# Performance work log

Measured on AMD Instinct MI355X. Metric: run time of the kernel, lower is better.

Reference implementation:

```python
import jax, jax.numpy as jnp
import numpy as np

NU = 100000  # num user nodes
NI = 100000  # num item nodes
E = 1600000  # edges per edge type
L = 100000   # labeled edges
H = 128      # hidden_channels
EPS = 1e-12  # F.normalize eps


def sage_conv(x_src, x_dst, edge_index, w_l, b_l, w_r, num_dst):
    """PyG SAGEConv, mean aggregation, normalize=True.
    w_l, w_r: [H, H] stored as [in, out]; lin_r has no bias."""
    src, dst = edge_index[0], edge_index[1]
    msg_sum = jax.ops.segment_sum(x_src[src], dst, num_segments=num_dst)  # [num_dst, H]
    cnt = jax.ops.segment_sum(jnp.ones((src.shape[0],), x_src.dtype), dst, num_segments=num_dst)
    mean = msg_sum / jnp.maximum(cnt, 1.0)[:, None]
    out = mean @ w_l + b_l + x_dst @ w_r
    norm = jnp.sqrt(jnp.sum(out * out, axis=-1, keepdims=True))
    return out / jnp.maximum(norm, EPS)


def setup_inputs() -> dict:
    key = jax.random.key(0)
    ks = jax.random.split(key, 20)
    s = 1.0 / np.sqrt(H)
    d = {
        'emb_user': jax.random.normal(ks[0], (NU, H), jnp.float32),
        'emb_item': jax.random.normal(ks[1], (NI, H), jnp.float32),
        'edge_rates': jax.random.randint(ks[2], (2, E), 0, 100000, jnp.int32),
        'edge_rev': jax.random.randint(ks[3], (2, E), 0, 100000, jnp.int32),
        'edge_label_index': jax.random.randint(ks[4], (2, L), 0, 100000, jnp.int32),
    }
    names = ['w1l_rates', 'w1r_rates', 'w1l_rev', 'w1r_rev',
             'w2l_rates', 'w2r_rates', 'w2l_rev', 'w2r_rev']
    for i, n in enumerate(names):
        d[n] = jax.random.uniform(ks[5 + i], (H, H), jnp.float32, -s, s)
    for i, n in enumerate(['b1_rates', 'b1_rev', 'b2_rates', 'b2_rev']):
        d[n] = jax.random.uniform(ks[13 + i], (H,), jnp.float32, -s, s)
    return d


def reference(emb_user, emb_item, edge_rates, edge_rev, edge_label_index,
              w1l_rates, w1r_rates, w1l_rev, w1r_rev,
              w2l_rates, w2r_rates, w2l_rev, w2r_rev,
              b1_rates, b1_rev, b2_rates, b2_rev):
    xu, xi = emb_user, emb_item
    # layer 1: each node type receives exactly one edge type (HeteroConv mean is identity)
    xi1 = sage_conv(xu, xi, edge_rates, w1l_rates, b1_rates, w1r_rates, NI)
    xu1 = sage_conv(xi, xu, edge_rev, w1l_rev, b1_rev, w1r_rev, NU)
    xu1 = jax.nn.relu(xu1)  # dropout is identity in eval mode
    xi1 = jax.nn.relu(xi1)
    # layer 2
    xi2 = sage_conv(xu1, xi1, edge_rates, w2l_rates, b2_rates, w2r_rates, NI)
    xu2 = sage_conv(xi1, xu1, edge_rev, w2l_rev, b2_rev, w2r_rev, NU)
    xu2 = jax.nn.relu(xu2)
    xi2 = jax.nn.relu(xi2)
    # classifier: dot(user[src], item[dst])
    x_src = xu2[edge_label_index[0]]
    x_dst = xi2[edge_label_index[1]]
    return jnp.sum(x_src * x_dst, axis=-1)
```

## Files before the change

kernel.cpp:

```cpp
#include <hip/hip_runtime.h>
#include <hip/hip_bf16.h>

#define NUM_U 100000
#define NUM_I 100000
#define NE    1600000
#define NL    100000
#define CAP   48
#define NBIN  391
#define BINCAP 4608
#define ROUND  4096
#define PB    391

typedef __attribute__((ext_vector_type(4))) float floatx4;
typedef __attribute__((ext_vector_type(8))) short shortx8;
typedef __attribute__((ext_vector_type(4))) unsigned uintx4;
typedef unsigned long long u64;

__device__ __forceinline__ float bf_lo(unsigned v) { return __uint_as_float(v << 16); }
__device__ __forceinline__ float bf_hi(unsigned v) { return __uint_as_float(v & 0xffff0000u); }

__device__ __forceinline__ unsigned pack_bf16x2(float lo, float hi) {
    __hip_bfloat16 l = __float2bfloat16(lo);
    __hip_bfloat16 h = __float2bfloat16(hi);
    unsigned short ul = *(unsigned short*)&l;
    unsigned short uh = *(unsigned short*)&h;
    return (unsigned)ul | ((unsigned)uh << 16);
}

__device__ __forceinline__ int clampi(int x, int hi) {
    return min(max(x, 0), hi - 1);
}

__global__ void prep1_kernel(
    const float* __restrict__ w1l_rates, const float* __restrict__ w1r_rates,
    const float* __restrict__ w1l_rev,   const float* __restrict__ w1r_rev,
    const float* __restrict__ w2l_rates, const float* __restrict__ w2r_rates,
    const float* __restrict__ w2l_rev,   const float* __restrict__ w2r_rev,
    short* __restrict__ Bt, int* __restrict__ bin_cursor,
    float* __restrict__ tailp, int ntail) {
    int idx = blockIdx.x * blockDim.x + threadIdx.x;
    if (idx < 2 * NBIN) bin_cursor[idx] = 0;
    if (idx < 4 * 32768) {
        int which = idx >> 15;
        int r = idx & 32767;
        int n = r >> 8;
        int k = r & 255;
        const float *wl, *wr;
        switch (which) {
            case 0:  wl = w1l_rates; wr = w1r_rates; break;
            case 1:  wl = w1l_rev;   wr = w1r_rev;   break;
            case 2:  wl = w2l_rates; wr = w2r_rates; break;
            default: wl = w2l_rev;   wr = w2r_rev;   break;
        }
        float v = (k < 128) ? wl[k * 128 + n] : wr[(k - 128) * 128 + n];
        __hip_bfloat16 b = __float2bfloat16(v);
        Bt[idx] = *(const short*)&b;
    } else {
        int t = idx - 4 * 32768;
        if (t < ntail) tailp[t] = 0.0f;
    }
}

__global__ __launch_bounds__(256) void prep2_kernel(
    const int* __restrict__ edges0, const int* __restrict__ edges1,
    u64* __restrict__ bd0, u64* __restrict__ bd1, int* __restrict__ cur,
    const float* __restrict__ emb_u, const float* __restrict__ emb_i,
    unsigned* __restrict__ xu, unsigned* __restrict__ xi) {
    __shared__ int hist[NBIN];
    __shared__ int prefix[NBIN];
    __shared__ int gbase[NBIN];
    __shared__ __align__(16) u64 sorted[ROUND];

    if (blockIdx.x >= 2 * PB) {
        int i = (blockIdx.x - 2 * PB) * blockDim.x + threadIdx.x;
        const int nu = NUM_U * 64;
        if (i < nu) {
            float2 v = ((const float2*)emb_u)[i];
            xu[i] = pack_bf16x2(v.x, v.y);
        } else if (i < nu + NUM_I * 64) {
            int j = i - nu;
            float2 v = ((const float2*)emb_i)[j];
            xi[j] = pack_bf16x2(v.x, v.y);
        }
        return;
    }

    const int type = (blockIdx.x >= PB) ? 1 : 0;
    const int* edges = type ? edges1 : edges0;
    u64* bin_data = type ? bd1 : bd0;
    int* bin_cursor = cur + type * NBIN;
    const int blk  = blockIdx.x - type * PB;
    const int tid  = threadIdx.x;
    const int lane = tid & 63;
    const int wv   = tid >> 6;
    const int base = blk * ROUND;

    for (int k = tid; k < NBIN; k += 256) hist[k] = 0;
    __syncthreads();

    int mybin[16], myrank[16], mysrc[16], mydst[16];
#pragma unroll
    for (int r = 0; r < 16; r++) {
        int i = base + r * 256 + tid;
        mybin[r] = -1;
        if (i < NE) {
            mysrc[r] = clampi(edges[i], NUM_U);
            mydst[r] = clampi(edges[i + NE], NUM_I);
            mybin[r] = mydst[r] >> 8;
            myrank[r] = atomicAdd(&hist[mybin[r]], 1);
        }
    }
    __syncthreads();

    if (wv == 0) {
        int carry = 0;
        for (int c = 0; c < NBIN; c += 64) {
            int idx = c + lane;
            int h = (idx < NBIN) ? hist[idx] : 0;
            int v = h;
            for (int o = 1; o < 64; o <<= 1) {
                int t = __shfl_up(v, o);
                if (lane >= o) v += t;
            }
            if (idx < NBIN) prefix[idx] = v - h + carry;
            carry += __shfl(v, 63);
        }
    }
    __syncthreads();

#pragma unroll
    for (int r = 0; r < 16; r++) {
        if (mybin[r] >= 0) {
            int j = prefix[mybin[r]] + myrank[r];
            sorted[j] = ((u64)(unsigned)mydst[r] << 32) | (unsigned)mysrc[r];
        }
    }
    __syncthreads();

    for (int b = tid; b < NBIN; b += 256) {
        int cnt = hist[b];
        gbase[b] = (cnt > 0) ? atomicAdd(&bin_cursor[b], cnt) : 0;
    }
    __syncthreads();

    int total = min(ROUND, NE - base);
    for (int j = tid; j < total; j += 256) {
        u64 e = sorted[j];
        int b = (int)(e >> 40);
        int pos = gbase[b] + (j - prefix[b]);
        if (pos < BINCAP)
            bin_data[(size_t)b * BINCAP + pos] = e;
    }
}

__global__ __launch_bounds__(256) void binscatter2_kernel(
    const u64* __restrict__ bd0, const u64* __restrict__ bd1, const int* __restrict__ cur,
    int* __restrict__ deg0, int* __restrict__ bucket0,
    int* __restrict__ deg1, int* __restrict__ bucket1) {
    __shared__ int lbucket[256 * CAP];
    __shared__ int ldeg[256];
    const int type = (blockIdx.x >= NBIN) ? 1 : 0;
    const int b = blockIdx.x - type * NBIN;
    const u64* bin_data = type ? bd1 : bd0;
    int* deg = type ? deg1 : deg0;
    int* bucket = type ? bucket1 : bucket0;
    const int tid = threadIdx.x;
    const int dstbase = b << 8;
    const int n_dst = NUM_I;

    ldeg[tid] = 0;
    __syncthreads();

    int count = min(cur[type * NBIN + b], BINCAP);
    for (int j = tid; j < count; j += 256) {
        u64 e = bin_data[(size_t)b * BINCAP + j];
        int src = (int)(unsigned)e;
        int dl = ((int)(e >> 32)) & 255;
        int pos = atomicAdd(&ldeg[dl], 1);
        if (pos < CAP) lbucket[dl * CAP + pos] = src;
    }
    __syncthreads();

    if (dstbase + tid < n_dst) deg[dstbase + tid] = ldeg[tid];
    int limit = min(256, n_dst - dstbase) * CAP;
    for (int k = tid; k < limit; k += 256)
        bucket[(size_t)dstbase * CAP + k] = lbucket[k];
}

__global__ __launch_bounds__(256) void agg2_kernel(
    const int* __restrict__ degA, const int* __restrict__ bucketA,
    const unsigned* __restrict__ xA, unsigned* __restrict__ outA,
    const int* __restrict__ degB, const int* __restrict__ bucketB,
    const unsigned* __restrict__ xB, unsigned* __restrict__ outB) {
    const int bid = blockIdx.x;
    const int g = bid & 7;
    const int typeB = (g >= 4);
    const int gidx = (bid >> 3) * 4 + (g & 3);
    const int node = gidx * 4 + (threadIdx.x >> 6);
    const int lane = threadIdx.x & 63;
    if (node >= NUM_I) return;

    const int* deg; const int* bucket; const unsigned* xb; unsigned* mo;
    if (!typeB) { deg = degA; bucket = bucketA; xb = xA; mo = outA; }
    else        { deg = degB; bucket = bucketB; xb = xB; mo = outB; }

    int d = __builtin_nontemporal_load(&deg[node]);
    int cnt = min(d, CAP);
    int srcs = (lane < cnt) ? __builtin_nontemporal_load(&bucket[(size_t)node * CAP + lane]) : 0;
    float a0 = 0.f, a1 = 0.f;
    int e = 0;
    for (; e + 8 <= cnt; e += 8) {
        int s0 = __builtin_amdgcn_readlane(srcs, e + 0);
        int s1 = __builtin_amdgcn_readlane(srcs, e + 1);
        int s2 = __builtin_amdgcn_readlane(srcs, e + 2);
        int s3 = __builtin_amdgcn_readlane(srcs, e + 3);
        int s4 = __builtin_amdgcn_readlane(srcs, e + 4);
        int s5 = __builtin_amdgcn_readlane(srcs, e + 5);
        int s6 = __builtin_amdgcn_readlane(srcs, e + 6);
        int s7 = __builtin_amdgcn_readlane(srcs, e + 7);
        unsigned v0 = xb[(size_t)s0 * 64 + lane];
        unsigned v1 = xb[(size_t)s1 * 64 + lane];
        unsigned v2 = xb[(size_t)s2 * 64 + lane];
        unsigned v3 = xb[(size_t)s3 * 64 + lane];
        unsigned v4 = xb[(size_t)s4 * 64 + lane];
        unsigned v5 = xb[(size_t)s5 * 64 + lane];
        unsigned v6 = xb[(size_t)s6 * 64 + lane];
        unsigned v7 = xb[(size_t)s7 * 64 + lane];
        a0 += bf_lo(v0) + bf_lo(v1) + bf_lo(v2) + bf_lo(v3)
            + bf_lo(v4) + bf_lo(v5) + bf_lo(v6) + bf_lo(v7);
        a1 += bf_hi(v0) + bf_hi(v1) + bf_hi(v2) + bf_hi(v3)
            + bf_hi(v4) + bf_hi(v5) + bf_hi(v6) + bf_hi(v7);
    }
    for (; e + 4 <= cnt; e += 4) {
        int s0 = __builtin_amdgcn_readlane(srcs, e + 0);
        int s1 = __builtin_amdgcn_readlane(srcs, e + 1);
        int s2 = __builtin_amdgcn_readlane(srcs, e + 2);
        int s3 = __builtin_amdgcn_readlane(srcs, e + 3);
        unsigned v0 = xb[(size_t)s0 * 64 + lane];
        unsigned v1 = xb[(size_t)s1 * 64 + lane];
        unsigned v2 = xb[(size_t)s2 * 64 + lane];
        unsigned v3 = xb[(size_t)s3 * 64 + lane];
        a0 += bf_lo(v0) + bf_lo(v1) + bf_lo(v2) + bf_lo(v3);
        a1 += bf_hi(v0) + bf_hi(v1) + bf_hi(v2) + bf_hi(v3);
    }
    for (; e < cnt; e++) {
        int s0 = __builtin_amdgcn_readlane(srcs, e);
        unsigned v0 = xb[(size_t)s0 * 64 + lane];
        a0 += bf_lo(v0); a1 += bf_hi(v0);
    }
    float scale = 1.0f / (float)max(d, 1);
    __builtin_nontemporal_store(pack_bf16x2(a0 * scale, a1 * scale),
                                &mo[(size_t)node * 64 + lane]);
}

__global__ __launch_bounds__(256) void gemm2r_kernel(
    const unsigned* __restrict__ meanA, unsigned* __restrict__ xA,
    const short* __restrict__ BtA, const float* __restrict__ biasA,
    const unsigned* __restrict__ meanB, unsigned* __restrict__ xB,
    const short* __restrict__ BtB, const float* __restrict__ biasB,
    int nblocksA) {
    __shared__ float rowsum[128][2];

    const int half = (blockIdx.x >= nblocksA) ? 1 : 0;
    const unsigned* meanb = half ? meanB : meanA;
    const unsigned* xdstb = half ? xB : xA;
    unsigned* outb = half ? xB : xA;
    const short* Bt = half ? BtB : BtA;
    const float* bias = half ? biasB : biasA;
    const int rb = (blockIdx.x - half * nblocksA) * 128;
    const int n_rows = NUM_I;

    const int tid  = threadIdx.x;
    const int lane = tid & 63;
    const int wv   = tid >> 6;
    const int wm   = wv >> 1;
    const int wn   = wv & 1;
    const int l15  = lane & 15;
    const int lq   = lane >> 4;

    floatx4 acc[4][4];
#pragma unroll
    for (int nt = 0; nt < 4; nt++) {
        float b = bias[wn * 64 + nt * 16 + l15];
#pragma unroll
        for (int mt = 0; mt < 4; mt++) acc[mt][nt] = (floatx4){b, b, b, b};
    }

    for (int kt = 0; kt < 4; kt++) {
        const unsigned* srcbuf = (kt < 2) ? meanb : xdstb;
        const int kbase_u = (kt & 1) * 32;
        uintx4 a8[4][2];
#pragma unroll
        for (int mt = 0; mt < 4; mt++) {
#pragma unroll
            for (int kk2 = 0; kk2 < 2; kk2++) {
                int grow = rb + wm * 64 + mt * 16 + l15;
                uintx4 v = (uintx4){0u, 0u, 0u, 0u};
                if (grow < n_rows)
                    v = *(const uintx4*)(srcbuf + (size_t)grow * 64 + kbase_u + kk2 * 16 + lq * 4);
                a8[mt][kk2] = v;
            }
        }
#pragma unroll
        for (int kk2 = 0; kk2 < 2; kk2++) {
            shortx8 bfr[4];
#pragma unroll
            for (int nt = 0; nt < 4; nt++) {
                int col = wn * 64 + nt * 16 + l15;
                int kg = kt * 64 + kk2 * 32 + lq * 8;
                bfr[nt] = *(const shortx8*)(Bt + col * 256 + kg);
            }
#pragma unroll
            for (int mt = 0; mt < 4; mt++)
#pragma unroll
                for (int nt = 0; nt < 4; nt++)
                    acc[mt][nt] = __builtin_amdgcn_mfma_f32_16x16x32_bf16(
                        *(const shortx8*)&a8[mt][kk2], bfr[nt], acc[mt][nt], 0, 0, 0);
        }
    }

#pragma unroll
    for (int mt = 0; mt < 4; mt++) {
#pragma unroll
        for (int r = 0; r < 4; r++) {
            float p = 0.f;
#pragma unroll
            for (int nt = 0; nt < 4; nt++) { float x = acc[mt][nt][r]; p += x * x; }
            for (int o = 1; o < 16; o <<= 1) p += __shfl_xor(p, o);
            if (l15 == 0) rowsum[wm * 64 + mt * 16 + lq * 4 + r][wn] = p;
        }
    }
    __syncthreads();

#pragma unroll
    for (int mt = 0; mt < 4; mt++) {
#pragma unroll
        for (int r = 0; r < 4; r++) {
            int row_l = wm * 64 + mt * 16 + lq * 4 + r;
            int grow = rb + row_l;
            float s = rowsum[row_l][0] + rowsum[row_l][1];
            float inv = 1.f / fmaxf(sqrtf(s), 1e-12f);
#pragma unroll
            for (int nt = 0; nt < 4; nt++) {
                float v = fmaxf(acc[mt][nt][r] * inv, 0.f);
                float vnb = __shfl_xor(v, 1);
                if (grow < n_rows && (l15 & 1) == 0) {
                    int colpair = (wn * 64 + nt * 16 + l15) >> 1;
                    outb[(size_t)grow * 64 + colpair] = pack_bf16x2(v, vnb);
                }
            }
        }
    }
}

__global__ __launch_bounds__(256) void classifier_kernel(
    const unsigned* __restrict__ xu, const unsigned* __restrict__ xi,
    const int* __restrict__ eli, float* __restrict__ out, int nL) {
    int wave = (blockIdx.x * blockDim.x + threadIdx.x) >> 6;
    int lane = threadIdx.x & 63;
    if (wave >= nL) return;
    int su = clampi(eli[wave], NUM_U);
    int di = clampi(eli[wave + nL], NUM_I);
    unsigned a = xu[(size_t)su * 64 + lane];
    unsigned b = xi[(size_t)di * 64 + lane];
    float p = bf_lo(a) * bf_lo(b) + bf_hi(a) * bf_hi(b);
    for (int o = 32; o; o >>= 1) p += __shfl_xor(p, o);
    if (lane == 0) __builtin_nontemporal_store(p, &out[wave]);
}

extern "C" void kernel_launch(void* const* d_in, const int* in_sizes, int n_in,
                              void* d_out, int out_size, void* d_ws, size_t ws_size,
                              hipStream_t stream) {
    const float* emb_user = (const float*)d_in[0];
    const float* emb_item = (const float*)d_in[1];
    const int* edge_rates = (const int*)d_in[2];
    const int* edge_rev   = (const int*)d_in[3];
    const int* eli        = (const int*)d_in[4];
    const float* b1_rates = (const float*)d_in[13];
    const float* b1_rev   = (const float*)d_in[14];
    const float* b2_rates = (const float*)d_in[15];
    const float* b2_rev   = (const float*)d_in[16];

    char* p = (char*)d_ws;
    auto alloc = [&](size_t bytes) -> void* {
        void* q = (void*)p;
        p += (bytes + 511) & ~(size_t)511;
        return q;
    };
    int* deg_rates    = (int*)alloc((size_t)NUM_I * 4);
    int* bucket_rates = (int*)alloc((size_t)NUM_I * CAP * 4);
    int* deg_rev      = (int*)alloc((size_t)NUM_U * 4);
    int* bucket_rev   = (int*)alloc((size_t)NUM_U * CAP * 4);
    unsigned* meanI = (unsigned*)alloc((size_t)NUM_I * 64 * 4);
    unsigned* meanU = (unsigned*)alloc((size_t)NUM_U * 64 * 4);
    unsigned* xi    = (unsigned*)alloc((size_t)NUM_I * 64 * 4);
    unsigned* xu    = (unsigned*)alloc((size_t)NUM_U * 64 * 4);
    short* Bt = (short*)alloc((size_t)4 * 32768 * 2);
    int* bin_cursor = (int*)alloc((size_t)2 * NBIN * 4);
    u64* bd0 = (u64*)meanI;
    u64* bd1 = (u64*)meanU;

    const int gemmBlocks = (NUM_I + 127) / 128;
    const int agg2Blocks = 2 * ((NUM_I + 3) / 4);
    const int conv2Blocks = ((NUM_U + NUM_I) * 64 + 255) / 256;

    const int ntail = (out_size > NL) ? (out_size - NL) : 0;
    const int prep1Blocks = 512 + (ntail + 255) / 256;
    const int prep2Blocks = 2 * PB + conv2Blocks;

    prep1_kernel<<<prep1Blocks, 256, 0, stream>>>(
        (const float*)d_in[5], (const float*)d_in[6],
        (const float*)d_in[7], (const float*)d_in[8],
        (const float*)d_in[9], (const float*)d_in[10],
        (const float*)d_in[11], (const float*)d_in[12], Bt, bin_cursor,
        (float*)d_out + NL, ntail);
    prep2_kernel<<<prep2Blocks, 256, 0, stream>>>(edge_rates, edge_rev, bd0, bd1, bin_cursor,
                                                  emb_user, emb_item, xu, xi);
    binscatter2_kernel<<<2 * NBIN, 256, 0, stream>>>(bd0, bd1, bin_cursor,
                                                     deg_rates, bucket_rates,
                                                     deg_rev, bucket_rev);

    agg2_kernel<<<agg2Blocks, 256, 0, stream>>>(deg_rates, bucket_rates, xu, meanI,
                                                deg_rev, bucket_rev, xi, meanU);
    gemm2r_kernel<<<2 * gemmBlocks, 256, 0, stream>>>(meanI, xi, Bt + 0 * 32768, b1_rates,
                                                      meanU, xu, Bt + 1 * 32768, b1_rev,
                                                      gemmBlocks);

    agg2_kernel<<<agg2Blocks, 256, 0, stream>>>(deg_rates, bucket_rates, xu, meanI,
                                                deg_rev, bucket_rev, xi, meanU);
    gemm2r_kernel<<<2 * gemmBlocks, 256, 0, stream>>>(meanI, xi, Bt + 2 * 32768, b2_rates,
                                                      meanU, xu, Bt + 3 * 32768, b2_rev,
                                                      gemmBlocks);

    classifier_kernel<<<(NL * 64 + 255) / 256, 256, 0, stream>>>(xu, xi, eli,
                                                                 (float*)d_out, NL);
}
```

Baseline: 638.1 us.

## Interleave aggregation and GEMM blocks in one kernel to overlap gather and MFMA phases

Merges the neighbour-mean gather and the SAGE linear/normalize GEMM into one kernel whose blocks are interleaved (one GEMM block per 17). The four aggregations and four GEMMs are reordered into a five-launch software pipeline, so each GEMM runs alongside the next aggregation, using ping-pong feature buffers. The GEMM tile drops to 64 rows with a full 128-column wave tile, which removes the shared-memory row-sum reduction. The embedding conversion is split out from the edge partition kernel. This trades extra buffers and careful dependency ordering for overlap of the memory-bound gather with compute-bound MFMA work.

Result: slower. 794.6 us (+24.5%).

```diff
diff --git a/kernel.cpp b/kernel.cpp
--- a/kernel.cpp
+++ b/kernel.cpp
@@ -10,6 +10,9 @@
 #define BINCAP 4608
 #define ROUND  4096
 #define PB    391
+#define NAGG  25000
+#define NGEMM 1563
+#define ILV   17
 
 typedef __attribute__((ext_vector_type(4))) float floatx4;
 typedef __attribute__((ext_vector_type(8))) short shortx8;
@@ -61,29 +64,27 @@
     }
 }
 
-__global__ __launch_bounds__(256) void prep2_kernel(
+__global__ void conv2_kernel(const float* __restrict__ emb_u, const float* __restrict__ emb_i,
+                             unsigned* __restrict__ xu, unsigned* __restrict__ xi) {
+    int i = blockIdx.x * blockDim.x + threadIdx.x;
+    const int nu = NUM_U * 64;
+    if (i < nu) {
+        float2 v = ((const float2*)emb_u)[i];
+        xu[i] = pack_bf16x2(v.x, v.y);
+    } else if (i < nu + NUM_I * 64) {
+        int j = i - nu;
+        float2 v = ((const float2*)emb_i)[j];
+        xi[j] = pack_bf16x2(v.x, v.y);
+    }
+}
+
+__global__ __launch_bounds__(256) void partition2_kernel(
     const int* __restrict__ edges0, const int* __restrict__ edges1,
-    u64* __restrict__ bd0, u64* __restrict__ bd1, int* __restrict__ cur,
-    const float* __restrict__ emb_u, const float* __restrict__ emb_i,
-    unsigned* __restrict__ xu, unsigned* __restrict__ xi) {
+    u64* __restrict__ bd0, u64* __restrict__ bd1, int* __restrict__ cur) {
     __shared__ int hist[NBIN];
     __shared__ int prefix[NBIN];
     __shared__ int gbase[NBIN];
     __shared__ __align__(16) u64 sorted[ROUND];
-
-    if (blockIdx.x >= 2 * PB) {
-        int i = (blockIdx.x - 2 * PB) * blockDim.x + threadIdx.x;
-        const int nu = NUM_U * 64;
-        if (i < nu) {
-            float2 v = ((const float2*)emb_u)[i];
-            xu[i] = pack_bf16x2(v.x, v.y);
-        } else if (i < nu + NUM_I * 64) {
-            int j = i - nu;
-            float2 v = ((const float2*)emb_i)[j];
-            xi[j] = pack_bf16x2(v.x, v.y);
-        }
-        return;
-    }
 
     const int type = (blockIdx.x >= PB) ? 1 : 0;
     const int* edges = type ? edges1 : edges0;
@@ -187,22 +188,73 @@
         bucket[(size_t)dstbase * CAP + k] = lbucket[k];
 }
 
-__global__ __launch_bounds__(256) void agg2_kernel(
-    const int* __restrict__ degA, const int* __restrict__ bucketA,
-    const unsigned* __restrict__ xA, unsigned* __restrict__ outA,
-    const int* __restrict__ degB, const int* __restrict__ bucketB,
-    const unsigned* __restrict__ xB, unsigned* __restrict__ outB) {
+__global__ __launch_bounds__(256, 8) void ag_kernel(
+    int nAgg, int nGemm,
+    const int* __restrict__ deg, const int* __restrict__ bucket,
+    const unsigned* __restrict__ xsrc, unsigned* __restrict__ mout,
+    const unsigned* __restrict__ gmean, const unsigned* __restrict__ gxdst,
+    const short* __restrict__ gBt, const float* __restrict__ gbias,
+    unsigned* __restrict__ gout) {
     const int bid = blockIdx.x;
-    const int g = bid & 7;
-    const int typeB = (g >= 4);
-    const int gidx = (bid >> 3) * 4 + (g & 3);
-    const int node = gidx * 4 + (threadIdx.x >> 6);
-    const int lane = threadIdx.x & 63;
+    int gemmIdx = -1, aggIdx = -1;
+    if (nGemm == 0) aggIdx = bid;
+    else if (nAgg == 0) gemmIdx = bid;
+    else {
+        int q = bid / ILV, r = bid - q * ILV;
+        if (r == 0 && q < nGemm) gemmIdx = q;
+        else aggIdx = bid - min(q + (r ? 1 : 0), nGemm);
+    }
+
+    const int tid  = threadIdx.x;
+    const int lane = tid & 63;
+    const int wv   = tid >> 6;
+    const int l15  = lane & 15;
+    const int lq   = lane >> 4;
+
+    if (gemmIdx >= 0) {
+        const int rb = gemmIdx * 64;
+        floatx4 acc[8];
+#pragma unroll
+        for (int nt = 0; nt < 8; nt++) {
+            float b = gbias[nt * 16 + l15];
+            acc[nt] = (floatx4){b, b, b, b};
+        }
+        const int grow = rb + wv * 16 + l15;
+#pragma unroll
+        for (int kt = 0; kt < 8; kt++) {
+            const unsigned* srcbuf = (kt < 4) ? gmean : gxdst;
+            uintx4 av = (uintx4){0u, 0u, 0u, 0u};
+            if (grow < NUM_I)
+                av = *(const uintx4*)(srcbuf + (size_t)grow * 64 + (kt & 3) * 16 + lq * 4);
+            shortx8 af = *(const shortx8*)&av;
+#pragma unroll
+            for (int nt = 0; nt < 8; nt++) {
+                shortx8 bfr = *(const shortx8*)(gBt + (nt * 16 + l15) * 256 + kt * 32 + lq * 8);
+                acc[nt] = __builtin_amdgcn_mfma_f32_16x16x32_bf16(af, bfr, acc[nt], 0, 0, 0);
+            }
+        }
+#pragma unroll
+        for (int r = 0; r < 4; r++) {
+            float p = 0.f;
+#pragma unroll
+            for (int nt = 0; nt < 8; nt++) { float x = acc[nt][r]; p += x * x; }
+            p += __shfl_xor(p, 1); p += __shfl_xor(p, 2);
+            p += __shfl_xor(p, 4); p += __shfl_xor(p, 8);
+            float inv = 1.f / fmaxf(sqrtf(p), 1e-12f);
+            int grow_out = rb + wv * 16 + lq * 4 + r;
+#pragma unroll
+            for (int nt = 0; nt < 8; nt++) {
+                float v = fmaxf(acc[nt][r] * inv, 0.f);
+                float vnb = __shfl_xor(v, 1);
+                if (grow_out < NUM_I && (l15 & 1) == 0)
+                    gout[(size_t)grow_out * 64 + ((nt * 16 + l15) >> 1)] = pack_bf16x2(v, vnb);
+            }
+        }
+        return;
+    }
+
+    const int node = aggIdx * 4 + wv;
     if (node >= NUM_I) return;
-
-    const int* deg; const int* bucket; const unsigned* xb; unsigned* mo;
-    if (!typeB) { deg = degA; bucket = bucketA; xb = xA; mo = outA; }
-    else        { deg = degB; bucket = bucketB; xb = xB; mo = outB; }
 
     int d = __builtin_nontemporal_load(&deg[node]);
     int cnt = min(d, CAP);
@@ -218,14 +270,14 @@
         int s5 = __builtin_amdgcn_readlane(srcs, e + 5);
         int s6 = __builtin_amdgcn_readlane(srcs, e + 6);
         int s7 = __builtin_amdgcn_readlane(srcs, e + 7);
-        unsigned v0 = xb[(size_t)s0 * 64 + lane];
-        unsigned v1 = xb[(size_t)s1 * 64 + lane];
-        unsigned v2 = xb[(size_t)s2 * 64 + lane];
-        unsigned v3 = xb[(size_t)s3 * 64 + lane];
-        unsigned v4 = xb[(size_t)s4 * 64 + lane];
-        unsigned v5 = xb[(size_t)s5 * 64 + lane];
-        unsigned v6 = xb[(size_t)s6 * 64 + lane];
-        unsigned v7 = xb[(size_t)s7 * 64 + lane];
+        unsigned v0 = xsrc[(size_t)s0 * 64 + lane];
+        unsigned v1 = xsrc[(size_t)s1 * 64 + lane];
+        unsigned v2 = xsrc[(size_t)s2 * 64 + lane];
+        unsigned v3 = xsrc[(size_t)s3 * 64 + lane];
+        unsigned v4 = xsrc[(size_t)s4 * 64 + lane];
+        unsigned v5 = xsrc[(size_t)s5 * 64 + lane];
+        unsigned v6 = xsrc[(size_t)s6 * 64 + lane];
+        unsigned v7 = xsrc[(size_t)s7 * 64 + lane];
         a0 += bf_lo(v0) + bf_lo(v1) + bf_lo(v2) + bf_lo(v3)
             + bf_lo(v4) + bf_lo(v5) + bf_lo(v6) + bf_lo(v7);
         a1 += bf_hi(v0) + bf_hi(v1) + bf_hi(v2) + bf_hi(v3)
@@ -236,121 +288,21 @@
         int s1 = __builtin_amdgcn_readlane(srcs, e + 1);
         int s2 = __builtin_amdgcn_readlane(srcs, e + 2);
         int s3 = __builtin_amdgcn_readlane(srcs, e + 3);
-        unsigned v0 = xb[(size_t)s0 * 64 + lane];
-        unsigned v1 = xb[(size_t)s1 * 64 + lane];
-        unsigned v2 = xb[(size_t)s2 * 64 + lane];
-        unsigned v3 = xb[(size_t)s3 * 64 + lane];
+        unsigned v0 = xsrc[(size_t)s0 * 64 + lane];
+        unsigned v1 = xsrc[(size_t)s1 * 64 + lane];
+        unsigned v2 = xsrc[(size_t)s2 * 64 + lane];
+        unsigned v3 = xsrc[(size_t)s3 * 64 + lane];
         a0 += bf_lo(v0) + bf_lo(v1) + bf_lo(v2) + bf_lo(v3);
         a1 += bf_hi(v0) + bf_hi(v1) + bf_hi(v2) + bf_hi(v3);
     }
     for (; e < cnt; e++) {
         int s0 = __builtin_amdgcn_readlane(srcs, e);
-        unsigned v0 = xb[(size_t)s0 * 64 + lane];
+        unsigned v0 = xsrc[(size_t)s0 * 64 + lane];
         a0 += bf_lo(v0); a1 += bf_hi(v0);
     }
     float scale = 1.0f / (float)max(d, 1);
     __builtin_nontemporal_store(pack_bf16x2(a0 * scale, a1 * scale),
-                                &mo[(size_t)node * 64 + lane]);
-}
-
-__global__ __launch_bounds__(256) void gemm2r_kernel(
-    const unsigned* __restrict__ meanA, unsigned* __restrict__ xA,
-    const short* __restrict__ BtA, const float* __restrict__ biasA,
-    const unsigned* __restrict__ meanB, unsigned* __restrict__ xB,
-    const short* __restrict__ BtB, const float* __restrict__ biasB,
-    int nblocksA) {
-    __shared__ float rowsum[128][2];
-
-    const int half = (blockIdx.x >= nblocksA) ? 1 : 0;
-    const unsigned* meanb = half ? meanB : meanA;
-    const unsigned* xdstb = half ? xB : xA;
-    unsigned* outb = half ? xB : xA;
-    const short* Bt = half ? BtB : BtA;
-    const float* bias = half ? biasB : biasA;
-    const int rb = (blockIdx.x - half * nblocksA) * 128;
-    const int n_rows = NUM_I;
-
-    const int tid  = threadIdx.x;
-    const int lane = tid & 63;
-    const int wv   = tid >> 6;
-    const int wm   = wv >> 1;
-    const int wn   = wv & 1;
-    const int l15  = lane & 15;
-    const int lq   = lane >> 4;
-
-    floatx4 acc[4][4];
-#pragma unroll
-    for (int nt = 0; nt < 4; nt++) {
-        float b = bias[wn * 64 + nt * 16 + l15];
-#pragma unroll
-        for (int mt = 0; mt < 4; mt++) acc[mt][nt] = (floatx4){b, b, b, b};
-    }
-
-    for (int kt = 0; kt < 4; kt++) {
-        const unsigned* srcbuf = (kt < 2) ? meanb : xdstb;
-        const int kbase_u = (kt & 1) * 32;
-        uintx4 a8[4][2];
-#pragma unroll
-        for (int mt = 0; mt < 4; mt++) {
-#pragma unroll
-            for (int kk2 = 0; kk2 < 2; kk2++) {
-                int grow = rb + wm * 64 + mt * 16 + l15;
-                uintx4 v = (uintx4){0u, 0u, 0u, 0u};
-                if (grow < n_rows)
-                    v = *(const uintx4*)(srcbuf + (size_t)grow * 64 + kbase_u + kk2 * 16 + lq * 4);
-                a8[mt][kk2] = v;
-            }
-        }
-#pragma unroll
-        for (int kk2 = 0; kk2 < 2; kk2++) {
-            shortx8 bfr[4];
-#pragma unroll
-            for (int nt = 0; nt < 4; nt++) {
-                int col = wn * 64 + nt * 16 + l15;
-                int kg = kt * 64 + kk2 * 32 + lq * 8;
-                bfr[nt] = *(const shortx8*)(Bt + col * 256 + kg);
-            }
-#pragma unroll
-            for (int mt = 0; mt < 4; mt++)
-#pragma unroll
-                for (int nt = 0; nt < 4; nt++)
-                    acc[mt][nt] = __builtin_amdgcn_mfma_f32_16x16x32_bf16(
-                        *(const shortx8*)&a8[mt][kk2], bfr[nt], acc[mt][nt], 0, 0, 0);
-        }
-    }
-
-#pragma unroll
-    for (int mt = 0; mt < 4; mt++) {
-#pragma unroll
-        for (int r = 0; r < 4; r++) {
-            float p = 0.f;
-#pragma unroll
-            for (int nt = 0; nt < 4; nt++) { float x = acc[mt][nt][r]; p += x * x; }
-            for (int o = 1; o < 16; o <<= 1) p += __shfl_xor(p, o);
-            if (l15 == 0) rowsum[wm * 64 + mt * 16 + lq * 4 + r][wn] = p;
-        }
-    }
-    __syncthreads();
-
-#pragma unroll
-    for (int mt = 0; mt < 4; mt++) {
-#pragma unroll
-        for (int r = 0; r < 4; r++) {
-            int row_l = wm * 64 + mt * 16 + lq * 4 + r;
-            int grow = rb + row_l;
-            float s = rowsum[row_l][0] + rowsum[row_l][1];
-            float inv = 1.f / fmaxf(sqrtf(s), 1e-12f);
-#pragma unroll
-            for (int nt = 0; nt < 4; nt++) {
-                float v = fmaxf(acc[mt][nt][r] * inv, 0.f);
-                float vnb = __shfl_xor(v, 1);
-                if (grow < n_rows && (l15 & 1) == 0) {
-                    int colpair = (wn * 64 + nt * 16 + l15) >> 1;
-                    outb[(size_t)grow * 64 + colpair] = pack_bf16x2(v, vnb);
-                }
-            }
-        }
-    }
+                                &mout[(size_t)node * 64 + lane]);
 }
 
 __global__ __launch_bounds__(256) void classifier_kernel(
@@ -391,22 +343,22 @@
     int* bucket_rates = (int*)alloc((size_t)NUM_I * CAP * 4);
     int* deg_rev      = (int*)alloc((size_t)NUM_U * 4);
     int* bucket_rev   = (int*)alloc((size_t)NUM_U * CAP * 4);
-    unsigned* meanI = (unsigned*)alloc((size_t)NUM_I * 64 * 4);
-    unsigned* meanU = (unsigned*)alloc((size_t)NUM_U * 64 * 4);
-    unsigned* xi    = (unsigned*)alloc((size_t)NUM_I * 64 * 4);
-    unsigned* xu    = (unsigned*)alloc((size_t)NUM_U * 64 * 4);
+    unsigned* M1  = (unsigned*)alloc((size_t)NUM_I * 64 * 4);
+    unsigned* M2  = (unsigned*)alloc((size_t)NUM_U * 64 * 4);
+    unsigned* xi0 = (unsigned*)alloc((size_t)NUM_I * 64 * 4);
+    unsigned* xu0 = (unsigned*)alloc((size_t)NUM_U * 64 * 4);
+    unsigned* xi1 = (unsigned*)alloc((size_t)NUM_I * 64 * 4);
+    unsigned* xu1 = (unsigned*)alloc((size_t)NUM_U * 64 * 4);
     short* Bt = (short*)alloc((size_t)4 * 32768 * 2);
     int* bin_cursor = (int*)alloc((size_t)2 * NBIN * 4);
-    u64* bd0 = (u64*)meanI;
-    u64* bd1 = (u64*)meanU;
-
-    const int gemmBlocks = (NUM_I + 127) / 128;
-    const int agg2Blocks = 2 * ((NUM_I + 3) / 4);
+    u64* bd0 = (u64*)M1;
+    u64* bd1 = (u64*)M2;
+    unsigned* M3 = xi0;
+
     const int conv2Blocks = ((NUM_U + NUM_I) * 64 + 255) / 256;
-
     const int ntail = (out_size > NL) ? (out_size - NL) : 0;
     const int prep1Blocks = 512 + (ntail + 255) / 256;
-    const int prep2Blocks = 2 * PB + conv2Blocks;
+    const int agBlocks = NAGG + NGEMM;
 
     prep1_kernel<<<prep1Blocks, 256, 0, stream>>>(
         (const float*)d_in[5], (const float*)d_in[6],
@@ -414,24 +366,28 @@
         (const float*)d_in[9], (const float*)d_in[10],
         (const float*)d_in[11], (const float*)d_in[12], Bt, bin_cursor,
         (float*)d_out + NL, ntail);
-    prep2_kernel<<<prep2Blocks, 256, 0, stream>>>(edge_rates, edge_rev, bd0, bd1, bin_cursor,
-                                                  emb_user, emb_item, xu, xi);
+    conv2_kernel<<<conv2Blocks, 256, 0, stream>>>(emb_user, emb_item, xu0, xi0);
+    partition2_kernel<<<2 * PB, 256, 0, stream>>>(edge_rates, edge_rev, bd0, bd1, bin_cursor);
     binscatter2_kernel<<<2 * NBIN, 256, 0, stream>>>(bd0, bd1, bin_cursor,
                                                      deg_rates, bucket_rates,
                                                      deg_rev, bucket_rev);
 
-    agg2_kernel<<<agg2Blocks, 256, 0, stream>>>(deg_rates, bucket_rates, xu, meanI,
-                                                deg_rev, bucket_rev, xi, meanU);
-    gemm2r_kernel<<<2 * gemmBlocks, 256, 0, stream>>>(meanI, xi, Bt + 0 * 32768, b1_rates,
-                                                      meanU, xu, Bt + 1 * 32768, b1_rev,
-                                                      gemmBlocks);
-
-    agg2_kernel<<<agg2Blocks, 256, 0, stream>>>(deg_rates, bucket_rates, xu, meanI,
-                                                deg_rev, bucket_rev, xi, meanU);
-    gemm2r_kernel<<<2 * gemmBlocks, 256, 0, stream>>>(meanI, xi, Bt + 2 * 32768, b2_rates,
-                                                      meanU, xu, Bt + 3 * 32768, b2_rev,
-                                                      gemmBlocks);
-
-    classifier_kernel<<<(NL * 64 + 255) / 256, 256, 0, stream>>>(xu, xi, eli,
+    ag_kernel<<<NAGG, 256, 0, stream>>>(NAGG, 0,
+        deg_rates, bucket_rates, xu0, M1,
+        M1, xi0, Bt, b1_rates, xi1);
+    ag_kernel<<<agBlocks, 256, 0, stream>>>(NAGG, NGEMM,
+        deg_rev, bucket_rev, xi0, M2,
+        M1, xi0, Bt + 0 * 32768, b1_rates, xi1);
+    ag_kernel<<<agBlocks, 256, 0, stream>>>(NAGG, NGEMM,
+        deg_rev, bucket_rev, xi1, M3,
+        M2, xu0, Bt + 1 * 32768, b1_rev, xu1);
+    ag_kernel<<<agBlocks, 256, 0, stream>>>(NAGG, NGEMM,
+        deg_rates, bucket_rates, xu1, M1,
+        M3, xu1, Bt + 3 * 32768, b2_rev, xu0);
+    ag_kernel<<<NGEMM, 256, 0, stream>>>(0, NGEMM,
+        deg_rates, bucket_rates, xu1, M1,
+        M1, xi1, Bt + 2 * 32768, b2_rates, xi0);
+
+    classifier_kernel<<<(NL * 64 + 255) / 256, 256, 0, stream>>>(xu0, xi0, eli,
                                                                  (float*)d_out, NL);
 }
```

## Use per-wave full-row GEMM tiles and split conversion out of partition kernel

Applied to the files above, without the earlier changes.

The GEMM+normalize kernel is retiled so each wave owns 16 full rows across all 128 output columns. The row L2 norm can then be reduced entirely with in-wave shuffles, removing the shared-memory rowsum and block barrier, at the cost of less A-fragment reuse across N and more B loads per wave. Separately, the embedding fp32-to-bf16 conversion is moved out of the edge-partition kernel into its own launch. This adds a kernel launch but gives the partition kernel a simpler, uniform grid.

New measurement: 692.1 us. 8.5% more time.

```diff
diff --git a/kernel.cpp b/kernel.cpp
--- a/kernel.cpp
+++ b/kernel.cpp
@@ -61,29 +61,27 @@
     }
 }
 
-__global__ __launch_bounds__(256) void prep2_kernel(
+__global__ void conv2_kernel(const float* __restrict__ emb_u, const float* __restrict__ emb_i,
+                             unsigned* __restrict__ xu, unsigned* __restrict__ xi) {
+    int i = blockIdx.x * blockDim.x + threadIdx.x;
+    const int nu = NUM_U * 64;
+    if (i < nu) {
+        float2 v = ((const float2*)emb_u)[i];
+        xu[i] = pack_bf16x2(v.x, v.y);
+    } else if (i < nu + NUM_I * 64) {
+        int j = i - nu;
+        float2 v = ((const float2*)emb_i)[j];
+        xi[j] = pack_bf16x2(v.x, v.y);
+    }
+}
+
+__global__ __launch_bounds__(256) void partition2_kernel(
     const int* __restrict__ edges0, const int* __restrict__ edges1,
-    u64* __restrict__ bd0, u64* __restrict__ bd1, int* __restrict__ cur,
-    const float* __restrict__ emb_u, const float* __restrict__ emb_i,
-    unsigned* __restrict__ xu, unsigned* __restrict__ xi) {
+    u64* __restrict__ bd0, u64* __restrict__ bd1, int* __restrict__ cur) {
     __shared__ int hist[NBIN];
     __shared__ int prefix[NBIN];
     __shared__ int gbase[NBIN];
     __shared__ __align__(16) u64 sorted[ROUND];
-
-    if (blockIdx.x >= 2 * PB) {
-        int i = (blockIdx.x - 2 * PB) * blockDim.x + threadIdx.x;
-        const int nu = NUM_U * 64;
-        if (i < nu) {
-            float2 v = ((const float2*)emb_u)[i];
-            xu[i] = pack_bf16x2(v.x, v.y);
-        } else if (i < nu + NUM_I * 64) {
-            int j = i - nu;
-            float2 v = ((const float2*)emb_i)[j];
-            xi[j] = pack_bf16x2(v.x, v.y);
-        }
-        return;
-    }
 
     const int type = (blockIdx.x >= PB) ? 1 : 0;
     const int* edges = type ? edges1 : edges0;
@@ -253,102 +251,61 @@
                                 &mo[(size_t)node * 64 + lane]);
 }
 
-__global__ __launch_bounds__(256) void gemm2r_kernel(
+__global__ __launch_bounds__(256) void gemmw_kernel(
     const unsigned* __restrict__ meanA, unsigned* __restrict__ xA,
     const short* __restrict__ BtA, const float* __restrict__ biasA,
     const unsigned* __restrict__ meanB, unsigned* __restrict__ xB,
     const short* __restrict__ BtB, const float* __restrict__ biasB,
     int nblocksA) {
-    __shared__ float rowsum[128][2];
-
     const int half = (blockIdx.x >= nblocksA) ? 1 : 0;
     const unsigned* meanb = half ? meanB : meanA;
-    const unsigned* xdstb = half ? xB : xA;
-    unsigned* outb = half ? xB : xA;
+    unsigned* xb = half ? xB : xA;
     const short* Bt = half ? BtB : BtA;
     const float* bias = half ? biasB : biasA;
-    const int rb = (blockIdx.x - half * nblocksA) * 128;
-    const int n_rows = NUM_I;
-
-    const int tid  = threadIdx.x;
-    const int lane = tid & 63;
-    const int wv   = tid >> 6;
-    const int wm   = wv >> 1;
-    const int wn   = wv & 1;
+    const int rb = (blockIdx.x - half * nblocksA) * 64;
+
+    const int lane = threadIdx.x & 63;
+    const int wv   = threadIdx.x >> 6;
     const int l15  = lane & 15;
     const int lq   = lane >> 4;
 
-    floatx4 acc[4][4];
-#pragma unroll
-    for (int nt = 0; nt < 4; nt++) {
-        float b = bias[wn * 64 + nt * 16 + l15];
-#pragma unroll
-        for (int mt = 0; mt < 4; mt++) acc[mt][nt] = (floatx4){b, b, b, b};
-    }
-
-    for (int kt = 0; kt < 4; kt++) {
-        const unsigned* srcbuf = (kt < 2) ? meanb : xdstb;
-        const int kbase_u = (kt & 1) * 32;
-        uintx4 a8[4][2];
-#pragma unroll
-        for (int mt = 0; mt < 4; mt++) {
-#pragma unroll
-            for (int kk2 = 0; kk2 < 2; kk2++) {
-                int grow = rb + wm * 64 + mt * 16 + l15;
-                uintx4 v = (uintx4){0u, 0u, 0u, 0u};
-                if (grow < n_rows)
-                    v = *(const uintx4*)(srcbuf + (size_t)grow * 64 + kbase_u + kk2 * 16 + lq * 4);
-                a8[mt][kk2] = v;
-            }
-        }
-#pragma unroll
-        for (int kk2 = 0; kk2 < 2; kk2++) {
-            shortx8 bfr[4];
-#pragma unroll
-            for (int nt = 0; nt < 4; nt++) {
-                int col = wn * 64 + nt * 16 + l15;
-                int kg = kt * 64 + kk2 * 32 + lq * 8;
-                bfr[nt] = *(const shortx8*)(Bt + col * 256 + kg);
-            }
-#pragma unroll
-            for (int mt = 0; mt < 4; mt++)
-#pragma unroll
-                for (int nt = 0; nt < 4; nt++)
-                    acc[mt][nt] = __builtin_amdgcn_mfma_f32_16x16x32_bf16(
-                        *(const shortx8*)&a8[mt][kk2], bfr[nt], acc[mt][nt], 0, 0, 0);
-        }
-    }
-
-#pragma unroll
-    for (int mt = 0; mt < 4; mt++) {
-#pragma unroll
-        for (int r = 0; r < 4; r++) {
-            float p = 0.f;
-#pragma unroll
-            for (int nt = 0; nt < 4; nt++) { float x = acc[mt][nt][r]; p += x * x; }
-            for (int o = 1; o < 16; o <<= 1) p += __shfl_xor(p, o);
-            if (l15 == 0) rowsum[wm * 64 + mt * 16 + lq * 4 + r][wn] = p;
-        }
-    }
-    __syncthreads();
-
-#pragma unroll
-    for (int mt = 0; mt < 4; mt++) {
-#pragma unroll
-        for (int r = 0; r < 4; r++) {
-            int row_l = wm * 64 + mt * 16 + lq * 4 + r;
-            int grow = rb + row_l;
-            float s = rowsum[row_l][0] + rowsum[row_l][1];
-            float inv = 1.f / fmaxf(sqrtf(s), 1e-12f);
-#pragma unroll
-            for (int nt = 0; nt < 4; nt++) {
-                float v = fmaxf(acc[mt][nt][r] * inv, 0.f);
-                float vnb = __shfl_xor(v, 1);
-                if (grow < n_rows && (l15 & 1) == 0) {
-                    int colpair = (wn * 64 + nt * 16 + l15) >> 1;
-                    outb[(size_t)grow * 64 + colpair] = pack_bf16x2(v, vnb);
-                }
-            }
+    floatx4 acc[8];
+#pragma unroll
+    for (int nt = 0; nt < 8; nt++) {
+        float b = bias[nt * 16 + l15];
+        acc[nt] = (floatx4){b, b, b, b};
+    }
+
+    const int grow = rb + wv * 16 + l15;
+#pragma unroll
+    for (int kt = 0; kt < 8; kt++) {
+        const unsigned* srcbuf = (kt < 4) ? meanb : xb;
+        uintx4 av = (uintx4){0u, 0u, 0u, 0u};
+        if (grow < NUM_I)
+            av = *(const uintx4*)(srcbuf + (size_t)grow * 64 + (kt & 3) * 16 + lq * 4);
+        shortx8 af = *(const shortx8*)&av;
+#pragma unroll
+        for (int nt = 0; nt < 8; nt++) {
+            shortx8 bfr = *(const shortx8*)(Bt + (nt * 16 + l15) * 256 + kt * 32 + lq * 8);
+            acc[nt] = __builtin_amdgcn_mfma_f32_16x16x32_bf16(af, bfr, acc[nt], 0, 0, 0);
+        }
+    }
+
+#pragma unroll
+    for (int r = 0; r < 4; r++) {
+        float p = 0.f;
+#pragma unroll
+        for (int nt = 0; nt < 8; nt++) { float x = acc[nt][r]; p += x * x; }
+        p += __shfl_xor(p, 1); p += __shfl_xor(p, 2);
+        p += __shfl_xor(p, 4); p += __shfl_xor(p, 8);
+        float inv = 1.f / fmaxf(sqrtf(p), 1e-12f);
+        int grow_out = rb + wv * 16 + lq * 4 + r;
+#pragma unroll
+        for (int nt = 0; nt < 8; nt++) {
+            float v = fmaxf(acc[nt][r] * inv, 0.f);
+            float vnb = __shfl_xor(v, 1);
+            if (grow_out < NUM_I && (l15 & 1) == 0)
+                xb[(size_t)grow_out * 64 + ((nt * 16 + l15) >> 1)] = pack_bf16x2(v, vnb);
         }
     }
 }
@@ -400,13 +357,11 @@
     u64* bd0 = (u64*)meanI;
     u64* bd1 = (u64*)meanU;
 
-    const int gemmBlocks = (NUM_I + 127) / 128;
+    const int gemmBlocks = (NUM_I + 63) / 64;
     const int agg2Blocks = 2 * ((NUM_I + 3) / 4);
     const int conv2Blocks = ((NUM_U + NUM_I) * 64 + 255) / 256;
-
     const int ntail = (out_size > NL) ? (out_size - NL) : 0;
     const int prep1Blocks = 512 + (ntail + 255) / 256;
-    const int prep2Blocks = 2 * PB + conv2Blocks;
 
     prep1_kernel<<<prep1Blocks, 256, 0, stream>>>(
         (const float*)d_in[5], (const float*)d_in[6],
@@ -414,23 +369,23 @@
         (const float*)d_in[9], (const float*)d_in[10],
         (const float*)d_in[11], (const float*)d_in[12], Bt, bin_cursor,
         (float*)d_out + NL, ntail);
-    prep2_kernel<<<prep2Blocks, 256, 0, stream>>>(edge_rates, edge_rev, bd0, bd1, bin_cursor,
-                                                  emb_user, emb_item, xu, xi);
+    conv2_kernel<<<conv2Blocks, 256, 0, stream>>>(emb_user, emb_item, xu, xi);
+    partition2_kernel<<<2 * PB, 256, 0, stream>>>(edge_rates, edge_rev, bd0, bd1, bin_cursor);
     binscatter2_kernel<<<2 * NBIN, 256, 0, stream>>>(bd0, bd1, bin_cursor,
                                                      deg_rates, bucket_rates,
                                                      deg_rev, bucket_rev);
 
     agg2_kernel<<<agg2Blocks, 256, 0, stream>>>(deg_rates, bucket_rates, xu, meanI,
                                                 deg_rev, bucket_rev, xi, meanU);
-    gemm2r_kernel<<<2 * gemmBlocks, 256, 0, stream>>>(meanI, xi, Bt + 0 * 32768, b1_rates,
-                                                      meanU, xu, Bt + 1 * 32768, b1_rev,
-                                                      gemmBlocks);
+    gemmw_kernel<<<2 * gemmBlocks, 256, 0, stream>>>(meanI, xi, Bt + 0 * 32768, b1_rates,
+                                                     meanU, xu, Bt + 1 * 32768, b1_rev,
+                                                     gemmBlocks);
 
     agg2_kernel<<<agg2Blocks, 256, 0, stream>>>(deg_rates, bucket_rates, xu, meanI,
                                                 deg_rev, bucket_rev, xi, meanU);
-    gemm2r_kernel<<<2 * gemmBlocks, 256, 0, stream>>>(meanI, xi, Bt + 2 * 32768, b2_rates,
-                                                      meanU, xu, Bt + 3 * 32768, b2_rev,
-                                                      gemmBlocks);
+    gemmw_kernel<<<2 * gemmBlocks, 256, 0, stream>>>(meanI, xi, Bt + 2 * 32768, b2_rates,
+                                                     meanU, xu, Bt + 3 * 32768, b2_rev,
+                                                     gemmBlocks);
 
     classifier_kernel<<<(NL * 64 + 255) / 256, 256, 0, stream>>>(xu, xi, eli,
                                                                  (float*)d_out, NL);
```
